# Kernel tuning notes

Hardware: AMD Instinct MI355X
Metric: run time of the kernel (lower is better)

Reference implementation:

```python
import jax, jax.numpy as jnp
import numpy as np

K_WIN = 7  # temporal window size (odd)
EPS = 1e-5


def setup_inputs() -> dict:
    key = jax.random.key(0)
    ks = jax.random.split(key, 10)
    B, C, T, H, W = 8, 512, 32, 7, 7
    N, E = 8, 64  # heads, inter channels = C // N
    s = 0.02
    return {
        "x": jax.random.normal(ks[0], (B, C, T, H, W), jnp.float32),
        "gamma": jnp.ones((C,), jnp.float32),
        "beta": jnp.zeros((C,), jnp.float32),
        "Wq": jax.random.normal(ks[1], (N, E, C), jnp.float32) * s,
        "bq": jax.random.normal(ks[2], (N, E), jnp.float32) * s,
        "Wk": jax.random.normal(ks[3], (N, E, C), jnp.float32) * s,
        "bk": jax.random.normal(ks[4], (N, E), jnp.float32) * s,
        "Wv": jax.random.normal(ks[5], (N, E, C), jnp.float32) * s,
        "bv": jax.random.normal(ks[6], (N, E), jnp.float32) * s,
        "Wo": jax.random.normal(ks[7], (N, C, E), jnp.float32) * s,
        "bo": jax.random.normal(ks[8], (N, C), jnp.float32) * s,
    }


def reference(x, gamma, beta, Wq, bq, Wk, bk, Wv, bv, Wo, bo):
    B, C, T, H, W = x.shape
    K = K_WIN
    P = H * W          # spatial positions per frame
    L = K * P          # positions per temporal window

    # BatchNorm3d (training-mode batch stats over B,T,H,W)
    mean = jnp.mean(x, axis=(0, 2, 3, 4), keepdims=True)
    var = jnp.var(x, axis=(0, 2, 3, 4), keepdims=True)
    g = gamma[None, :, None, None, None]
    b = beta[None, :, None, None, None]
    xb = g * (x - mean) * jax.lax.rsqrt(var + EPS) + b  # (B,C,T,H,W)

    # temporal zero-pad so that number of windows S == T
    pad = K // 2
    xp = jnp.pad(xb, ((0, 0), (0, 0), (pad, pad), (0, 0), (0, 0)))
    # gather sliding windows: (B,C,T,K,H,W)
    win_idx = jnp.arange(T)[:, None] + jnp.arange(K)[None, :]
    xw = xp[:, :, win_idx]

    xwf = xw.reshape(B, C, T, L)   # window tokens (key/value source)
    xcf = xb.reshape(B, C, T, P)   # center frame (query source)

    # per-head projections (dropout is identity in eval mode)
    q = jnp.einsum('nec,bctp->bntep', Wq, xcf) + bq[None, :, None, :, None]
    k = jnp.einsum('nec,bctl->bntel', Wk, xwf) + bk[None, :, None, :, None]
    v = jnp.einsum('nec,bctl->bntel', Wv, xwf) + bv[None, :, None, :, None]

    # attention: scores (B,N,T,P,L), softmax over window positions L (no scaling, as in original)
    alpha = jnp.einsum('bntep,bntel->bntpl', q, k)
    alpha = jax.nn.softmax(alpha, axis=-1)
    y = jnp.einsum('bntpl,bntel->bntep', alpha, v)

    # output projection per head, then mean over heads
    out = jnp.einsum('nce,bntep->bntcp', Wo, y) + bo[None, :, None, :, None]
    z = jnp.mean(out, axis=1)                 # (B,T,C,P)
    z = jnp.transpose(z, (0, 2, 1, 3)).reshape(B, C, T, H, W)
    return z + xb  # residual with BN output
```

## Files before the change

kernel.cpp:

```cpp
#include <hip/hip_runtime.h>
#include <hip/hip_bf16.h>


typedef float f32x4 __attribute__((ext_vector_type(4)));
typedef float f32x2 __attribute__((ext_vector_type(2)));
typedef short s16x8 __attribute__((ext_vector_type(8)));
typedef short s16x4 __attribute__((ext_vector_type(4)));
typedef __bf16 bf16x8 __attribute__((ext_vector_type(8)));

static __device__ __forceinline__ float bf2f(unsigned short u){
  union { unsigned int i; float f; } x; x.i = ((unsigned int)u) << 16; return x.f;
}
static __device__ __forceinline__ unsigned short f2bf(float f){
  union { __hip_bfloat16 h; unsigned short u; } x; x.h = __float2bfloat16(f); return x.u;
}
static __device__ __forceinline__ f32x4 mfma16(s16x8 a, s16x8 b, f32x4 c){
  return __builtin_amdgcn_mfma_f32_16x16x32_bf16(
      __builtin_bit_cast(bf16x8, a), __builtin_bit_cast(bf16x8, b), c, 0, 0, 0);
}
static __device__ __forceinline__ void gload16(const unsigned short* g, unsigned short* l){
  __builtin_amdgcn_global_load_lds(
      (const __attribute__((address_space(1))) unsigned int*)g,
      (__attribute__((address_space(3))) unsigned int*)l, 16, 0, 0);
}

__global__ __launch_bounds__(256) void xt_kernel(const float* __restrict__ x,
    unsigned short* __restrict__ Xt, float* __restrict__ partials){
  __shared__ unsigned short Xc[512][53];
  const int bt = blockIdx.x, b = bt >> 5, t = bt & 31, tid = threadIdx.x;
  const float* xb = x + (size_t)b*802816 + t*49;
  for (int i = tid; i < 512*49; i += 256){
    int c = i / 49, p = i - c*49;
    Xc[c][p] = f2bf(xb[(size_t)c*1568 + p]);
  }
  __syncthreads();
  unsigned short* dst = Xt + (size_t)bt*49*512;
  for (int i = tid; i < 49*64; i += 256){
    int p = i >> 6, c0 = (i & 63) << 3;
    s16x8 v;
    #pragma unroll
    for (int j = 0; j < 8; ++j) v[j] = (short)Xc[c0+j][p];
    *(s16x8*)(dst + p*512 + c0) = v;
  }
  for (int c = tid; c < 512; c += 256){
    float s1 = 0.f, s2 = 0.f;
    #pragma unroll 7
    for (int p = 0; p < 49; ++p){
      float f = bf2f(Xc[c][p]);
      s1 += f; s2 += f*f;
    }
    f32x2 o; o[0] = s1; o[1] = s2;
    *(f32x2*)(partials + ((size_t)bt*512 + c)*2) = o;
  }
}

__global__ __launch_bounds__(256) void stats2_kernel(const float* __restrict__ partials,
    const float* __restrict__ gamma, const float* __restrict__ beta,
    float* __restrict__ scale, float* __restrict__ shift){
  __shared__ float R1[4][64], R2[4][64];
  const int h = blockIdx.x, tid = threadIdx.x;
  const int r = tid >> 6, co = tid & 63;
  const int c = h*64 + co;
  float s1 = 0.f, s2 = 0.f;
  for (int k = r; k < 256; k += 4){
    f32x2 v = *(const f32x2*)(partials + ((size_t)k*512 + c)*2);
    s1 += v[0]; s2 += v[1];
  }
  R1[r][co] = s1; R2[r][co] = s2;
  __syncthreads();
  if (tid < 64){
    float t1 = R1[0][tid]+R1[1][tid]+R1[2][tid]+R1[3][tid];
    float t2 = R2[0][tid]+R2[1][tid]+R2[2][tid]+R2[3][tid];
    const int cc = h*64 + tid;
    const float inv = 1.f/12544.f;
    float mean = t1*inv;
    float var  = t2*inv - mean*mean;
    float sc = gamma[cc]*rsqrtf(var + 1e-5f);
    scale[cc] = sc;
    shift[cc] = beta[cc] - mean*sc;
  }
}

__global__ __launch_bounds__(512) void prep_kernel(const float* __restrict__ Wq,
    const float* __restrict__ Wk, const float* __restrict__ Wv,
    const float* __restrict__ Wo, const float* __restrict__ bo,
    const float* __restrict__ bq, const float* __restrict__ bk,
    const float* __restrict__ bv,
    const float* __restrict__ scale, const float* __restrict__ shift,
    unsigned short* __restrict__ Wall, unsigned short* __restrict__ Wo2,
    float* __restrict__ bo_sum, float* __restrict__ biasAll){
  const float L2E = 1.4426950408889634f;
  const int bid = blockIdx.x;
  if (bid < 2049){
    int i = bid*512 + threadIdx.x;
    if (i < 786432){
      const float* W = (i < 262144) ? Wq : (i < 524288 ? Wk : Wv);
      float m = (i < 262144) ? L2E : 1.f;
      Wall[i] = f2bf(W[i & 262143] * scale[i & 511] * m);
    } else if (i < 1048576){
      int j = i - 786432;
      int c = j >> 9, k = j & 511, nn = k >> 6, e = k & 63;
      Wo2[j] = f2bf(Wo[((size_t)nn*512 + c)*64 + e] * 0.125f);
    } else if (i < 1049088){
      int c = i - 1048576;
      float s = 0.f;
      #pragma unroll
      for (int nn = 0; nn < 8; ++nn) s += bo[nn*512 + c];
      bo_sum[c] = s * 0.125f;
    }
  } else {
    const int row = (bid - 2049)*8 + (threadIdx.x >> 6);
    const int lane = threadIdx.x & 63;
    const float* W    = row < 512 ? Wq : (row < 1024 ? Wk : Wv);
    const float* bsrc = row < 512 ? bq : (row < 1024 ? bk : bv);
    const int r = row & 511;
    const float* Wr = W + (size_t)r*512;
    float s = 0.f;
    #pragma unroll
    for (int j = 0; j < 8; ++j) s += Wr[lane + 64*j]*shift[lane + 64*j];
    #pragma unroll
    for (int off = 32; off > 0; off >>= 1) s += __shfl_down(s, off);
    if (lane == 0) biasAll[row] = (bsrc[r] + s) * (row < 512 ? L2E : 1.f);
  }
}

__global__ __launch_bounds__(256) void kv_gemm(const unsigned short* __restrict__ Wall,
    const unsigned short* __restrict__ Xt, const float* __restrict__ biasAll,
    unsigned short* __restrict__ Kg, unsigned short* __restrict__ Vg){
  __shared__ unsigned short As[2][4096];
  __shared__ unsigned short Bs[2][4096];
  const int bid = blockIdx.x;
  const int id = (bid & 7)*98 + (bid >> 3);
  const int bm = id & 7, bn = id >> 3;
  const int m0 = bm*128, n0 = bn*128;
  const int tid = threadIdx.x;
  const int w = __builtin_amdgcn_readfirstlane(tid >> 6);
  const int lane = tid & 63, l15 = lane & 15, g = lane >> 4, g4 = (lane >> 4)*4;
  const int wm = w >> 1, wn = w & 1;
  const int cA = w*128 + lane;
  int offA[4], offB[4];
  #pragma unroll
  for (int mi = 0; mi < 4; ++mi){
    int row = wm*64 + mi*16 + l15;
    offA[mi] = row*32 + ((g ^ ((row>>1)&3))<<3);
  }
  #pragma unroll
  for (int ni = 0; ni < 4; ++ni){
    int col = wn*64 + ni*16 + l15;
    offB[ni] = col*32 + ((g ^ ((col>>1)&3))<<3);
  }
  f32x4 acc[4][4];
  #pragma unroll
  for (int mi = 0; mi < 4; ++mi)
    #pragma unroll
    for (int ni = 0; ni < 4; ++ni) acc[mi][ni] = 0.f;

  const unsigned short* Akv = Wall + 512*512;
  auto stage = [&](int bufi, int ks){
    #pragma unroll
    for (int it = 0; it < 2; ++it){
      int c = cA + it*64;
      int row = c >> 2, slot = c & 3;
      int ko = ks*32 + ((slot ^ ((row>>1)&3))<<3);
      gload16(Akv + (size_t)(m0 + row)*512 + ko, &As[bufi][(w*128 + it*64)*8]);
      gload16(Xt  + (size_t)(n0 + row)*512 + ko, &Bs[bufi][(w*128 + it*64)*8]);
    }
  };
  auto compute = [&](int bufi){
    s16x8 Af[4], Bf[4];
    #pragma unroll
    for (int mi = 0; mi < 4; ++mi) Af[mi] = *(const s16x8*)&As[bufi][offA[mi]];
    #pragma unroll
    for (int ni = 0; ni < 4; ++ni) Bf[ni] = *(const s16x8*)&Bs[bufi][offB[ni]];
    #pragma unroll
    for (int mi = 0; mi < 4; ++mi)
      #pragma unroll
      for (int ni = 0; ni < 4; ++ni)
        acc[mi][ni] = mfma16(Af[mi], Bf[ni], acc[mi][ni]);
  };

  stage(0, 0);
  __syncthreads();
  #pragma unroll 1
  for (int kk = 0; kk < 8; ++kk){
    stage(1, kk*2 + 1);
    compute(0);
    __syncthreads();
    if (kk < 7) stage(0, kk*2 + 2);
    compute(1);
    __syncthreads();
  }

  const int qb = bm*2 + wm;
  const int which = qb >> 3, n = qb & 7;
  f32x4 bb[4];
  #pragma unroll
  for (int mi = 0; mi < 4; ++mi)
    bb[mi] = *(const f32x4*)(biasAll + 512 + qb*64 + mi*16 + g4);
  #pragma unroll
  for (int ni = 0; ni < 4; ++ni){
    const int col = n0 + wn*64 + ni*16 + l15;
    const int btc = col / 49, p = col - btc*49;
    const size_t bnt = ((size_t)((btc >> 5)*8 + n)*32 + (btc & 31));
    #pragma unroll
    for (int mi = 0; mi < 4; ++mi){
      const int e0 = mi*16 + g4;
      f32x4 v = acc[mi][ni] + bb[mi];
      if (which == 0){
        s16x4 u;
        #pragma unroll
        for (int r = 0; r < 4; ++r) u[r] = (short)f2bf(v[r]);
        *(s16x4*)(Kg + (bnt*49 + p)*64 + e0) = u;
      } else {
        #pragma unroll
        for (int r = 0; r < 4; ++r)
          Vg[bnt*3328 + (size_t)(e0 + r)*52 + p] = f2bf(v[r]);
      }
    }
  }
}

__global__ __launch_bounds__(512,2) void attn_fused(
    const unsigned short* __restrict__ Wall, const unsigned short* __restrict__ Wo2,
    const unsigned short* __restrict__ Xt,
    const unsigned short* __restrict__ Kg, const unsigned short* __restrict__ Vg,
    const float* __restrict__ biasAll, const float* __restrict__ bk,
    const float* __restrict__ bv, const float* __restrict__ scale,
    const float* __restrict__ shift, const float* __restrict__ bo_sum,
    float* __restrict__ out){
  __shared__ unsigned short Ls[64*512];
  const int bid = blockIdx.x;
  const int bt = ((bid & 7) << 5) | (bid >> 3);
  const int b = bt >> 5, t = bt & 31, tid = threadIdx.x;
  const int n = __builtin_amdgcn_readfirstlane(tid >> 6);
  const int lane = tid & 63, g = lane >> 4, l15 = lane & 15, g4 = (lane >> 4)*4;

  #pragma unroll
  for (int it = 0; it < 8; ++it){
    int s = it*512 + tid;
    int p = s >> 6, qs = s & 63;
    int qsrc = qs ^ (p & 7);
    int pc = p < 49 ? p : 48;
    gload16(Xt + ((size_t)(bt*49 + pc))*512 + qsrc*8, &Ls[s*8]);
  }
  asm volatile("s_waitcnt vmcnt(0)" ::: "memory");
  __syncthreads();

  f32x4 qacc[4][4];
  #pragma unroll
  for (int mi = 0; mi < 4; ++mi)
    #pragma unroll
    for (int ni = 0; ni < 4; ++ni) qacc[mi][ni] = 0.f;
  #pragma unroll 4
  for (int ks = 0; ks < 16; ++ks){
    s16x8 Bf[4];
    #pragma unroll
    for (int ni = 0; ni < 4; ++ni){
      int p = ni*16 + l15, q = ks*4 + g;
      Bf[ni] = *(const s16x8*)&Ls[p*512 + ((q ^ (p&7))<<3)];
    }
    #pragma unroll
    for (int mi = 0; mi < 4; ++mi){
      s16x8 Af = *(const s16x8*)(Wall + (size_t)(n*64 + mi*16 + l15)*512 + ks*32 + g*8);
      #pragma unroll
      for (int ni = 0; ni < 4; ++ni)
        qacc[mi][ni] = mfma16(Af, Bf[ni], qacc[mi][ni]);
    }
  }
  __syncthreads();

  #pragma unroll
  for (int mi = 0; mi < 4; ++mi){
    const int e = mi*16 + g4;
    const f32x4 bq4 = *(const f32x4*)(biasAll + n*64 + e);
    const int ne = n*64 + e, q = ne >> 3;
    #pragma unroll
    for (int ni = 0; ni < 4; ++ni){
      const int p = ni*16 + l15;
      f32x4 v = qacc[mi][ni] + bq4;
      s16x4 u;
      #pragma unroll
      for (int r = 0; r < 4; ++r) u[r] = (short)f2bf(v[r]);
      *(s16x4*)&Ls[p*512 + ((q ^ (p&7))<<3) + (ne & 7)] = u;
    }
  }
  s16x8 Qf[4][2];
  #pragma unroll
  for (int ni = 0; ni < 4; ++ni)
    #pragma unroll
    for (int ks = 0; ks < 2; ++ks){
      const int p = ni*16 + l15, q = n*8 + ks*4 + g;
      Qf[ni][ks] = *(const s16x8*)&Ls[p*512 + ((q ^ (p&7))<<3)];
    }

  const float* bkp = bk + n*64;
  f32x4 bkf[2][2];
  bkf[0][0] = *(const f32x4*)(bkp + g*8);      bkf[0][1] = *(const f32x4*)(bkp + g*8 + 4);
  bkf[1][0] = *(const f32x4*)(bkp + 32 + g*8); bkf[1][1] = *(const f32x4*)(bkp + 32 + g*8 + 4);
  float pad_l[4];
  #pragma unroll
  for (int ni = 0; ni < 4; ++ni){
    float s = 0.f;
    #pragma unroll
    for (int ks = 0; ks < 2; ++ks)
      #pragma unroll
      for (int h = 0; h < 2; ++h)
        #pragma unroll
        for (int j = 0; j < 4; ++j)
          s += bf2f((unsigned short)Qf[ni][ks][h*4+j]) * bkf[ks][h][j];
    s += __shfl_xor(s, 16); s += __shfl_xor(s, 32);
    pad_l[ni] = s;
  }
  float m_run[4], d_run[4];
  f32x4 Yacc[4][4];
  #pragma unroll
  for (int ni = 0; ni < 4; ++ni){
    m_run[ni] = -1e30f; d_run[ni] = 0.f;
    #pragma unroll
    for (int me = 0; me < 4; ++me) Yacc[me][ni] = 0.f;
  }
  int slo = 3 - t; if (slo < 0) slo = 0;
  int shi = 34 - t; if (shi > 6) shi = 6;
  for (int s = slo; s <= shi; ++s){
    const int tt = t + s - 3;
    const unsigned short* Kb = Kg + ((size_t)(b*8 + n)*32 + tt)*3136;
    const unsigned short* Vb = Vg + ((size_t)(b*8 + n)*32 + tt)*3328;
    f32x4 S[4][4];
    #pragma unroll
    for (int mi = 0; mi < 4; ++mi)
      #pragma unroll
      for (int ni = 0; ni < 4; ++ni) S[mi][ni] = 0.f;
    __builtin_amdgcn_s_setprio(1);
    #pragma unroll
    for (int ks = 0; ks < 2; ++ks)
      #pragma unroll
      for (int mi = 0; mi < 4; ++mi){
        s16x8 Kf = *(const s16x8*)(Kb + (mi*16 + l15)*64 + ks*32 + g*8);
        #pragma unroll
        for (int ni = 0; ni < 4; ++ni)
          S[mi][ni] = mfma16(Kf, Qf[ni][ks], S[mi][ni]);
      }
    __builtin_amdgcn_s_setprio(0);
    #pragma unroll
    for (int r = 0; r < 4; ++r){
      const bool bad = (g4 + r) >= 1;
      #pragma unroll
      for (int ni = 0; ni < 4; ++ni)
        S[3][ni][r] = bad ? -1e30f : S[3][ni][r];
    }
    #pragma unroll
    for (int ni = 0; ni < 4; ++ni){
      float mx = -1e30f;
      #pragma unroll
      for (int mi = 0; mi < 4; ++mi)
        #pragma unroll
        for (int r = 0; r < 4; ++r) mx = fmaxf(mx, S[mi][ni][r]);
      mx = fmaxf(mx, __shfl_xor(mx, 16));
      mx = fmaxf(mx, __shfl_xor(mx, 32));
      const float mn = fmaxf(m_run[ni], mx);
      const float rs = exp2f(m_run[ni] - mn);
      m_run[ni] = mn;
      float sum = 0.f;
      #pragma unroll
      for (int mi = 0; mi < 4; ++mi)
        #pragma unroll
        for (int r = 0; r < 4; ++r){
          float e = exp2f(S[mi][ni][r] - mn);
          S[mi][ni][r] = e; sum += e;
        }
      sum += __shfl_xor(sum, 16); sum += __shfl_xor(sum, 32);
      d_run[ni] = d_run[ni]*rs + sum;
      #pragma unroll
      for (int me = 0; me < 4; ++me) Yacc[me][ni] *= rs;
    }
    #pragma unroll
    for (int ks = 0; ks < 2; ++ks){
      s16x8 Pf[4];
      #pragma unroll
      for (int ni = 0; ni < 4; ++ni){
        f32x4 a = S[2*ks][ni], b2 = S[2*ks+1][ni];
        s16x8 pf;
        #pragma unroll
        for (int j = 0; j < 4; ++j){
          pf[j]   = (short)f2bf(a[j]);
          pf[4+j] = (short)f2bf(b2[j]);
        }
        Pf[ni] = pf;
      }
      __builtin_amdgcn_s_setprio(1);
      #pragma unroll
      for (int me = 0; me < 4; ++me){
        s16x4 vlo = *(const s16x4*)(Vb + (size_t)(me*16 + l15)*52 + ks*32 + g4);
        s16x4 vhi = *(const s16x4*)(Vb + (size_t)(me*16 + l15)*52 + ks*32 + 16 + g4);
        s16x8 Vf;
        #pragma unroll
        for (int j = 0; j < 4; ++j){ Vf[j] = vlo[j]; Vf[4+j] = vhi[j]; }
        #pragma unroll
        for (int ni = 0; ni < 4; ++ni)
          Yacc[me][ni] = mfma16(Vf, Pf[ni], Yacc[me][ni]);
      }
      __builtin_amdgcn_s_setprio(0);
    }
  }
  const int n_pad = slo + (6 - shi);
  f32x4 bvf[4];
  #pragma unroll
  for (int me = 0; me < 4; ++me)
    bvf[me] = *(const f32x4*)(bv + n*64 + me*16 + g4);
  #pragma unroll
  for (int ni = 0; ni < 4; ++ni){
    float rs = 1.f, pw = 0.f, d = d_run[ni];
    if (n_pad > 0){
      const float mf = fmaxf(m_run[ni], pad_l[ni]);
      rs = exp2f(m_run[ni] - mf);
      pw = (float)(n_pad*49) * exp2f(pad_l[ni] - mf);
      d = d_run[ni]*rs + pw;
    }
    const float inv = 1.f/d;
    const int p = ni*16 + l15;
    #pragma unroll
    for (int me = 0; me < 4; ++me){
      const int ne = n*64 + me*16 + g4, q = ne >> 3;
      s16x4 u;
      #pragma unroll
      for (int r = 0; r < 4; ++r)
        u[r] = (short)f2bf((Yacc[me][ni][r]*rs + pw*bvf[me][r])*inv);
      *(s16x4*)&Ls[p*512 + ((q ^ (p&7))<<3) + (ne & 7)] = u;
    }
  }
  __syncthreads();

  {
    f32x4 acc[4][4];
    #pragma unroll
    for (int mi = 0; mi < 4; ++mi)
      #pragma unroll
      for (int ni = 0; ni < 4; ++ni) acc[mi][ni] = 0.f;
    #pragma unroll 4
    for (int ks = 0; ks < 16; ++ks){
      s16x8 Bf[4];
      #pragma unroll
      for (int ni = 0; ni < 4; ++ni){
        int p = ni*16 + l15, q = ks*4 + g;
        Bf[ni] = *(const s16x8*)&Ls[p*512 + ((q ^ (p&7))<<3)];
      }
      #pragma unroll
      for (int mi = 0; mi < 4; ++mi){
        s16x8 Af = *(const s16x8*)(Wo2 + (size_t)(n*64 + mi*16 + l15)*512 + ks*32 + g*8);
        #pragma unroll
        for (int ni = 0; ni < 4; ++ni)
          acc[mi][ni] = mfma16(Af, Bf[ni], acc[mi][ni]);
      }
    }
    #pragma unroll
    for (int mi = 0; mi < 4; ++mi){
      const int c0 = n*64 + mi*16 + g4;
      const f32x4 bs = *(const f32x4*)(bo_sum + c0);
      const f32x4 sc = *(const f32x4*)(scale + c0);
      const f32x4 sh = *(const f32x4*)(shift + c0);
      #pragma unroll
      for (int ni = 0; ni < 4; ++ni){
        const int p = ni*16 + l15;
        if (p < 49){
          s16x4 xb = *(const s16x4*)(Xt + ((size_t)(bt*49 + p))*512 + c0);
          const size_t obase = (size_t)b*802816 + t*49 + p;
          #pragma unroll
          for (int r = 0; r < 4; ++r){
            out[obase + (size_t)(c0 + r)*1568] =
                acc[mi][ni][r] + bs[r] + sc[r]*bf2f((unsigned short)xb[r]) + sh[r];
          }
        }
      }
    }
  }
}

extern "C" void kernel_launch(void* const* d_in, const int* in_sizes, int n_in_,
                              void* d_out, int out_size, void* d_ws, size_t ws_size,
                              hipStream_t stream){
  const float* x     = (const float*)d_in[0];
  const float* gamma = (const float*)d_in[1];
  const float* beta  = (const float*)d_in[2];
  const float* Wq    = (const float*)d_in[3];
  const float* bq    = (const float*)d_in[4];
  const float* Wk    = (const float*)d_in[5];
  const float* bk    = (const float*)d_in[6];
  const float* Wv    = (const float*)d_in[7];
  const float* bv    = (const float*)d_in[8];
  const float* Wo    = (const float*)d_in[9];
  const float* bo    = (const float*)d_in[10];
  float* out = (float*)d_out;

  char* ws = (char*)d_ws;
  float* scale    = (float*)ws;
  float* shift    = scale + 512;
  float* bo_sum   = shift + 512;
  float* biasAll  = bo_sum + 512;
  float* partials = biasAll + 1536;
  unsigned short* Wall = (unsigned short*)(ws + 1064960);
  const size_t PAD = 16384;
  unsigned short* Wo2 = Wall + 786432;
  unsigned short* Xt  = Wo2 + 262144;
  unsigned short* Kg  = Xt + 6422528 + PAD;
  unsigned short* Vg  = Kg + 6422528 + PAD;

  hipLaunchKernelGGL(xt_kernel, dim3(256), dim3(256), 0, stream, x, Xt, partials);
  hipLaunchKernelGGL(stats2_kernel, dim3(8), dim3(256), 0, stream,
                     partials, gamma, beta, scale, shift);
  hipLaunchKernelGGL(prep_kernel, dim3(2241), dim3(512), 0, stream,
                     Wq, Wk, Wv, Wo, bo, bq, bk, bv, scale, shift,
                     Wall, Wo2, bo_sum, biasAll);
  hipLaunchKernelGGL(kv_gemm, dim3(784), dim3(256), 0, stream,
                     Wall, Xt, biasAll, Kg, Vg);
  hipLaunchKernelGGL(attn_fused, dim3(256), dim3(512), 0, stream,
                     Wall, Wo2, Xt, Kg, Vg, biasAll, bk, bv,
                     scale, shift, bo_sum, out);
}
```

Measured before the change: 147.9 us.

## Split attention blocks into 16-query quarters and permute K/Wo layouts

The fused attention kernel now processes 16 query positions per block instead of 64, so it launches 1024 blocks instead of 256 and uses a quarter of the LDS. Q stays in registers as the MFMA output fragment, with no LDS round trip. To make that possible, K and Wo2 are stored with a permuted head-dim order that matches the MFMA accumulator layout. The aim is better CU occupancy and less register and LDS pressure. The cost is that each block reloads the K/V windows and the Wq/Wo weight tiles for fewer queries, multiplying global/L2 traffic by four.

```diff
diff --git a/kernel.cpp b/kernel.cpp
--- a/kernel.cpp
+++ b/kernel.cpp
@@ -99,7 +99,8 @@
       Wall[i] = f2bf(W[i & 262143] * scale[i & 511] * m);
     } else if (i < 1048576){
       int j = i - 786432;
-      int c = j >> 9, k = j & 511, nn = k >> 6, e = k & 63;
+      int c = j >> 9, k = j & 511, nn = k >> 6, pos = k & 63;
+      int e = (2*(pos >> 5) + ((pos & 7) >> 2))*16 + ((pos >> 3) & 3)*4 + (pos & 3);
       Wo2[j] = f2bf(Wo[((size_t)nn*512 + c)*64 + e] * 0.125f);
     } else if (i < 1049088){
       int c = i - 1048576;
@@ -204,14 +205,15 @@
     const size_t bnt = ((size_t)((btc >> 5)*8 + n)*32 + (btc & 31));
     #pragma unroll
     for (int mi = 0; mi < 4; ++mi){
-      const int e0 = mi*16 + g4;
       f32x4 v = acc[mi][ni] + bb[mi];
       if (which == 0){
         s16x4 u;
         #pragma unroll
         for (int r = 0; r < 4; ++r) u[r] = (short)f2bf(v[r]);
-        *(s16x4*)(Kg + (bnt*49 + p)*64 + e0) = u;
+        const int kpos = (mi >> 1)*32 + g*8 + (mi & 1)*4;
+        *(s16x4*)(Kg + (bnt*49 + p)*64 + kpos) = u;
       } else {
+        const int e0 = mi*16 + g4;
         #pragma unroll
         for (int r = 0; r < 4; ++r)
           Vg[bnt*3328 + (size_t)(e0 + r)*52 + p] = f2bf(v[r]);
@@ -228,164 +230,121 @@
     const float* __restrict__ bv, const float* __restrict__ scale,
     const float* __restrict__ shift, const float* __restrict__ bo_sum,
     float* __restrict__ out){
-  __shared__ unsigned short Ls[64*512];
+  __shared__ unsigned short Ls[16*512];
   const int bid = blockIdx.x;
-  const int bt = ((bid & 7) << 5) | (bid >> 3);
+  const int id = (bid & 7)*128 + (bid >> 3);
+  const int bt = id >> 2, qr = id & 3;
   const int b = bt >> 5, t = bt & 31, tid = threadIdx.x;
   const int n = __builtin_amdgcn_readfirstlane(tid >> 6);
   const int lane = tid & 63, g = lane >> 4, l15 = lane & 15, g4 = (lane >> 4)*4;
-
-  #pragma unroll
-  for (int it = 0; it < 8; ++it){
-    int s = it*512 + tid;
-    int p = s >> 6, qs = s & 63;
-    int qsrc = qs ^ (p & 7);
-    int pc = p < 49 ? p : 48;
-    gload16(Xt + ((size_t)(bt*49 + pc))*512 + qsrc*8, &Ls[s*8]);
+  const int p0 = qr*16;
+
+  {
+    int s = tid;
+    #pragma unroll
+    for (int it = 0; it < 2; ++it, s += 512){
+      int pl = s >> 6, q = s & 63;
+      int pg = p0 + pl; if (pg > 48) pg = 48;
+      gload16(Xt + ((size_t)(bt*49 + pg))*512 + ((q ^ (pl & 7))<<3), &Ls[s*8]);
+    }
   }
   asm volatile("s_waitcnt vmcnt(0)" ::: "memory");
   __syncthreads();
 
-  f32x4 qacc[4][4];
-  #pragma unroll
-  for (int mi = 0; mi < 4; ++mi)
-    #pragma unroll
-    for (int ni = 0; ni < 4; ++ni) qacc[mi][ni] = 0.f;
+  f32x4 qacc[4];
+  #pragma unroll
+  for (int mi = 0; mi < 4; ++mi) qacc[mi] = 0.f;
   #pragma unroll 4
   for (int ks = 0; ks < 16; ++ks){
-    s16x8 Bf[4];
-    #pragma unroll
-    for (int ni = 0; ni < 4; ++ni){
-      int p = ni*16 + l15, q = ks*4 + g;
-      Bf[ni] = *(const s16x8*)&Ls[p*512 + ((q ^ (p&7))<<3)];
-    }
+    s16x8 Bf = *(const s16x8*)&Ls[l15*512 + (((ks*4 + g) ^ (l15 & 7))<<3)];
     #pragma unroll
     for (int mi = 0; mi < 4; ++mi){
       s16x8 Af = *(const s16x8*)(Wall + (size_t)(n*64 + mi*16 + l15)*512 + ks*32 + g*8);
-      #pragma unroll
-      for (int ni = 0; ni < 4; ++ni)
-        qacc[mi][ni] = mfma16(Af, Bf[ni], qacc[mi][ni]);
-    }
-  }
-  __syncthreads();
-
-  #pragma unroll
-  for (int mi = 0; mi < 4; ++mi){
-    const int e = mi*16 + g4;
-    const f32x4 bq4 = *(const f32x4*)(biasAll + n*64 + e);
-    const int ne = n*64 + e, q = ne >> 3;
-    #pragma unroll
-    for (int ni = 0; ni < 4; ++ni){
-      const int p = ni*16 + l15;
-      f32x4 v = qacc[mi][ni] + bq4;
-      s16x4 u;
-      #pragma unroll
-      for (int r = 0; r < 4; ++r) u[r] = (short)f2bf(v[r]);
-      *(s16x4*)&Ls[p*512 + ((q ^ (p&7))<<3) + (ne & 7)] = u;
-    }
-  }
-  s16x8 Qf[4][2];
-  #pragma unroll
-  for (int ni = 0; ni < 4; ++ni)
-    #pragma unroll
-    for (int ks = 0; ks < 2; ++ks){
-      const int p = ni*16 + l15, q = n*8 + ks*4 + g;
-      Qf[ni][ks] = *(const s16x8*)&Ls[p*512 + ((q ^ (p&7))<<3)];
-    }
-
-  const float* bkp = bk + n*64;
-  f32x4 bkf[2][2];
-  bkf[0][0] = *(const f32x4*)(bkp + g*8);      bkf[0][1] = *(const f32x4*)(bkp + g*8 + 4);
-  bkf[1][0] = *(const f32x4*)(bkp + 32 + g*8); bkf[1][1] = *(const f32x4*)(bkp + 32 + g*8 + 4);
-  float pad_l[4];
-  #pragma unroll
-  for (int ni = 0; ni < 4; ++ni){
+      qacc[mi] = mfma16(Af, Bf, qacc[mi]);
+    }
+  }
+  __syncthreads();
+
+  f32x4 q4[4];
+  float pad_l;
+  {
     float s = 0.f;
     #pragma unroll
-    for (int ks = 0; ks < 2; ++ks)
-      #pragma unroll
-      for (int h = 0; h < 2; ++h)
-        #pragma unroll
-        for (int j = 0; j < 4; ++j)
-          s += bf2f((unsigned short)Qf[ni][ks][h*4+j]) * bkf[ks][h][j];
+    for (int mi = 0; mi < 4; ++mi){
+      const f32x4 bb = *(const f32x4*)(biasAll + n*64 + mi*16 + g4);
+      q4[mi] = qacc[mi] + bb;
+      const f32x4 bkf = *(const f32x4*)(bk + n*64 + mi*16 + g4);
+      s += q4[mi][0]*bkf[0] + q4[mi][1]*bkf[1] + q4[mi][2]*bkf[2] + q4[mi][3]*bkf[3];
+    }
     s += __shfl_xor(s, 16); s += __shfl_xor(s, 32);
-    pad_l[ni] = s;
-  }
-  float m_run[4], d_run[4];
-  f32x4 Yacc[4][4];
-  #pragma unroll
-  for (int ni = 0; ni < 4; ++ni){
-    m_run[ni] = -1e30f; d_run[ni] = 0.f;
-    #pragma unroll
-    for (int me = 0; me < 4; ++me) Yacc[me][ni] = 0.f;
-  }
+    pad_l = s;
+  }
+  s16x8 Qbf[2];
+  #pragma unroll
+  for (int ks = 0; ks < 2; ++ks){
+    s16x8 pf;
+    #pragma unroll
+    for (int j = 0; j < 4; ++j){
+      pf[j]   = (short)f2bf(q4[2*ks][j]);
+      pf[4+j] = (short)f2bf(q4[2*ks+1][j]);
+    }
+    Qbf[ks] = pf;
+  }
+
+  float m_run = -1e30f, d_run = 0.f;
+  f32x4 Yacc[4];
+  #pragma unroll
+  for (int me = 0; me < 4; ++me) Yacc[me] = 0.f;
   int slo = 3 - t; if (slo < 0) slo = 0;
   int shi = 34 - t; if (shi > 6) shi = 6;
   for (int s = slo; s <= shi; ++s){
     const int tt = t + s - 3;
     const unsigned short* Kb = Kg + ((size_t)(b*8 + n)*32 + tt)*3136;
     const unsigned short* Vb = Vg + ((size_t)(b*8 + n)*32 + tt)*3328;
-    f32x4 S[4][4];
-    #pragma unroll
-    for (int mi = 0; mi < 4; ++mi)
-      #pragma unroll
-      for (int ni = 0; ni < 4; ++ni) S[mi][ni] = 0.f;
+    f32x4 S[4];
+    #pragma unroll
+    for (int mi = 0; mi < 4; ++mi) S[mi] = 0.f;
     __builtin_amdgcn_s_setprio(1);
     #pragma unroll
     for (int ks = 0; ks < 2; ++ks)
       #pragma unroll
       for (int mi = 0; mi < 4; ++mi){
         s16x8 Kf = *(const s16x8*)(Kb + (mi*16 + l15)*64 + ks*32 + g*8);
-        #pragma unroll
-        for (int ni = 0; ni < 4; ++ni)
-          S[mi][ni] = mfma16(Kf, Qf[ni][ks], S[mi][ni]);
+        S[mi] = mfma16(Kf, Qbf[ks], S[mi]);
       }
     __builtin_amdgcn_s_setprio(0);
     #pragma unroll
-    for (int r = 0; r < 4; ++r){
-      const bool bad = (g4 + r) >= 1;
-      #pragma unroll
-      for (int ni = 0; ni < 4; ++ni)
-        S[3][ni][r] = bad ? -1e30f : S[3][ni][r];
-    }
-    #pragma unroll
-    for (int ni = 0; ni < 4; ++ni){
-      float mx = -1e30f;
-      #pragma unroll
-      for (int mi = 0; mi < 4; ++mi)
-        #pragma unroll
-        for (int r = 0; r < 4; ++r) mx = fmaxf(mx, S[mi][ni][r]);
-      mx = fmaxf(mx, __shfl_xor(mx, 16));
-      mx = fmaxf(mx, __shfl_xor(mx, 32));
-      const float mn = fmaxf(m_run[ni], mx);
-      const float rs = exp2f(m_run[ni] - mn);
-      m_run[ni] = mn;
-      float sum = 0.f;
-      #pragma unroll
-      for (int mi = 0; mi < 4; ++mi)
-        #pragma unroll
-        for (int r = 0; r < 4; ++r){
-          float e = exp2f(S[mi][ni][r] - mn);
-          S[mi][ni][r] = e; sum += e;
-        }
-      sum += __shfl_xor(sum, 16); sum += __shfl_xor(sum, 32);
-      d_run[ni] = d_run[ni]*rs + sum;
-      #pragma unroll
-      for (int me = 0; me < 4; ++me) Yacc[me][ni] *= rs;
-    }
+    for (int r = 0; r < 4; ++r)
+      S[3][r] = ((g4 + r) >= 1) ? -1e30f : S[3][r];
+    float mx = -1e30f;
+    #pragma unroll
+    for (int mi = 0; mi < 4; ++mi)
+      #pragma unroll
+      for (int r = 0; r < 4; ++r) mx = fmaxf(mx, S[mi][r]);
+    mx = fmaxf(mx, __shfl_xor(mx, 16));
+    mx = fmaxf(mx, __shfl_xor(mx, 32));
+    const float mn = fmaxf(m_run, mx);
+    const float rs = exp2f(m_run - mn);
+    m_run = mn;
+    float sum = 0.f;
+    #pragma unroll
+    for (int mi = 0; mi < 4; ++mi)
+      #pragma unroll
+      for (int r = 0; r < 4; ++r){
+        float e = exp2f(S[mi][r] - mn);
+        S[mi][r] = e; sum += e;
+      }
+    sum += __shfl_xor(sum, 16); sum += __shfl_xor(sum, 32);
+    d_run = d_run*rs + sum;
+    #pragma unroll
+    for (int me = 0; me < 4; ++me) Yacc[me] *= rs;
     #pragma unroll
     for (int ks = 0; ks < 2; ++ks){
-      s16x8 Pf[4];
-      #pragma unroll
-      for (int ni = 0; ni < 4; ++ni){
-        f32x4 a = S[2*ks][ni], b2 = S[2*ks+1][ni];
-        s16x8 pf;
-        #pragma unroll
-        for (int j = 0; j < 4; ++j){
-          pf[j]   = (short)f2bf(a[j]);
-          pf[4+j] = (short)f2bf(b2[j]);
-        }
-        Pf[ni] = pf;
+      s16x8 Pf;
+      #pragma unroll
+      for (int j = 0; j < 4; ++j){
+        Pf[j]   = (short)f2bf(S[2*ks][j]);
+        Pf[4+j] = (short)f2bf(S[2*ks+1][j]);
       }
       __builtin_amdgcn_s_setprio(1);
       #pragma unroll
@@ -395,80 +354,61 @@
         s16x8 Vf;
         #pragma unroll
         for (int j = 0; j < 4; ++j){ Vf[j] = vlo[j]; Vf[4+j] = vhi[j]; }
-        #pragma unroll
-        for (int ni = 0; ni < 4; ++ni)
-          Yacc[me][ni] = mfma16(Vf, Pf[ni], Yacc[me][ni]);
+        Yacc[me] = mfma16(Vf, Pf, Yacc[me]);
       }
       __builtin_amdgcn_s_setprio(0);
     }
   }
-  const int n_pad = slo + (6 - shi);
-  f32x4 bvf[4];
-  #pragma unroll
-  for (int me = 0; me < 4; ++me)
-    bvf[me] = *(const f32x4*)(bv + n*64 + me*16 + g4);
-  #pragma unroll
-  for (int ni = 0; ni < 4; ++ni){
-    float rs = 1.f, pw = 0.f, d = d_run[ni];
+  {
+    const int n_pad = slo + (6 - shi);
+    float rs = 1.f, pw = 0.f, d = d_run;
     if (n_pad > 0){
-      const float mf = fmaxf(m_run[ni], pad_l[ni]);
-      rs = exp2f(m_run[ni] - mf);
-      pw = (float)(n_pad*49) * exp2f(pad_l[ni] - mf);
-      d = d_run[ni]*rs + pw;
+      const float mf = fmaxf(m_run, pad_l);
+      rs = exp2f(m_run - mf);
+      pw = (float)(n_pad*49) * exp2f(pad_l - mf);
+      d = d_run*rs + pw;
     }
     const float inv = 1.f/d;
-    const int p = ni*16 + l15;
     #pragma unroll
     for (int me = 0; me < 4; ++me){
-      const int ne = n*64 + me*16 + g4, q = ne >> 3;
+      const f32x4 bvf = *(const f32x4*)(bv + n*64 + me*16 + g4);
       s16x4 u;
       #pragma unroll
       for (int r = 0; r < 4; ++r)
-        u[r] = (short)f2bf((Yacc[me][ni][r]*rs + pw*bvf[me][r])*inv);
-      *(s16x4*)&Ls[p*512 + ((q ^ (p&7))<<3) + (ne & 7)] = u;
+        u[r] = (short)f2bf((Yacc[me][r]*rs + pw*bvf[r])*inv);
+      const int q = n*8 + (me >> 1)*4 + g;
+      *(s16x4*)&Ls[l15*512 + ((q ^ (l15 & 7))<<3) + (me & 1)*4] = u;
     }
   }
   __syncthreads();
 
   {
-    f32x4 acc[4][4];
-    #pragma unroll
-    for (int mi = 0; mi < 4; ++mi)
-      #pragma unroll
-      for (int ni = 0; ni < 4; ++ni) acc[mi][ni] = 0.f;
+    f32x4 acc[4];
+    #pragma unroll
+    for (int mi = 0; mi < 4; ++mi) acc[mi] = 0.f;
     #pragma unroll 4
     for (int ks = 0; ks < 16; ++ks){
-      s16x8 Bf[4];
-      #pragma unroll
-      for (int ni = 0; ni < 4; ++ni){
-        int p = ni*16 + l15, q = ks*4 + g;
-        Bf[ni] = *(const s16x8*)&Ls[p*512 + ((q ^ (p&7))<<3)];
-      }
+      s16x8 Bf = *(const s16x8*)&Ls[l15*512 + (((ks*4 + g) ^ (l15 & 7))<<3)];
       #pragma unroll
       for (int mi = 0; mi < 4; ++mi){
         s16x8 Af = *(const s16x8*)(Wo2 + (size_t)(n*64 + mi*16 + l15)*512 + ks*32 + g*8);
+        acc[mi] = mfma16(Af, Bf, acc[mi]);
+      }
+    }
+    const int p = p0 + l15;
+    if (p < 49){
+      #pragma unroll
+      for (int mi = 0; mi < 4; ++mi){
+        const int c0 = n*64 + mi*16 + g4;
+        const f32x4 bs = *(const f32x4*)(bo_sum + c0);
+        const f32x4 sc = *(const f32x4*)(scale + c0);
+        const f32x4 sh = *(const f32x4*)(shift + c0);
+        s16x4 xb = *(const s16x4*)(Xt + ((size_t)(bt*49 + p))*512 + c0);
+        const size_t obase = (size_t)b*802816 + t*49 + p;
         #pragma unroll
-        for (int ni = 0; ni < 4; ++ni)
-          acc[mi][ni] = mfma16(Af, Bf[ni], acc[mi][ni]);
-      }
-    }
-    #pragma unroll
-    for (int mi = 0; mi < 4; ++mi){
-      const int c0 = n*64 + mi*16 + g4;
-      const f32x4 bs = *(const f32x4*)(bo_sum + c0);
-      const f32x4 sc = *(const f32x4*)(scale + c0);
-      const f32x4 sh = *(const f32x4*)(shift + c0);
-      #pragma unroll
-      for (int ni = 0; ni < 4; ++ni){
-        const int p = ni*16 + l15;
-        if (p < 49){
-          s16x4 xb = *(const s16x4*)(Xt + ((size_t)(bt*49 + p))*512 + c0);
-          const size_t obase = (size_t)b*802816 + t*49 + p;
-          #pragma unroll
-          for (int r = 0; r < 4; ++r){
-            out[obase + (size_t)(c0 + r)*1568] =
-                acc[mi][ni][r] + bs[r] + sc[r]*bf2f((unsigned short)xb[r]) + sh[r];
-          }
+        for (int r = 0; r < 4; ++r){
+          out[obase + (size_t)(c0 + r)*1568] =
+              acc[mi][r] + bs[r] + sc[r]*bf2f((unsigned short)xb[r]) + sh[r];
         }
       }
     }
@@ -512,7 +452,7 @@
                      Wall, Wo2, bo_sum, biasAll);
   hipLaunchKernelGGL(kv_gemm, dim3(784), dim3(256), 0, stream,
                      Wall, Xt, biasAll, Kg, Vg);
-  hipLaunchKernelGGL(attn_fused, dim3(256), dim3(512), 0, stream,
+  hipLaunchKernelGGL(attn_fused, dim3(1024), dim3(512), 0, stream,
                      Wall, Wo2, Xt, Kg, Vg, biasAll, bk, bv,
                      scale, shift, bo_sum, out);
 }
```

Measured after the change: 277.8 us. 87.8% more time.
